# Performance work log

Measured on AMD Instinct MI355X. Metric: run time of the kernel, lower is better.

The kernel has to match this reference:

```python
import jax, jax.numpy as jnp
import numpy as np
import math

EPS = 1e-5  # BatchNorm eps; eval mode with running_mean=0, running_var=1


def maxpool(x, k, p):
    return jax.lax.reduce_window(x, -jnp.inf, jax.lax.max,
                                 (1, 1, k, k), (1, 1, 1, 1),
                                 ((0, 0), (0, 0), (p, p), (p, p)))


def conv1x1(x, w, b=None):
    # x: [B,Cin,H,W], w: [Cout,Cin]
    y = jnp.einsum('oi,bihw->bohw', w, x)
    if b is not None:
        y = y + b[None, :, None, None]
    return y


def bn_eval(x, g, b):
    scale = g / jnp.sqrt(1.0 + EPS)
    return x * scale[None, :, None, None] + b[None, :, None, None]


def setup_inputs() -> dict:
    B, C, H, W = 2, 64, 80, 80
    c1, c2, c3 = 21, 21, 22
    ch = 32  # C//2
    ks = jax.random.split(jax.random.key(0), 16)
    s = 0.05
    inp = {
        'x': jax.random.normal(ks[0], (B, C, H, W), jnp.float32),
        'q1_w': jax.random.normal(ks[1], (c1, c1), jnp.float32) * s,
        'q1_g': jnp.ones((c1,), jnp.float32),
        'q1_b': jnp.zeros((c1,), jnp.float32),
        'q2_w': jax.random.normal(ks[2], (c2, c2), jnp.float32) * s,
        'q2_g': jnp.ones((c2,), jnp.float32),
        'q2_b': jnp.zeros((c2,), jnp.float32),
        'q3_w': jax.random.normal(ks[3], (c3, c3), jnp.float32) * s,
        'q3_g': jnp.ones((c3,), jnp.float32),
        'q3_b': jnp.zeros((c3,), jnp.float32),
        'k_hf_w': jax.random.normal(ks[4], (ch, C), jnp.float32) * s,
        'k_hf_b': jnp.zeros((ch,), jnp.float32),
        'k_lf_w': jax.random.normal(ks[5], (C - ch, C), jnp.float32) * s,
        'k_lf_b': jnp.zeros((C - ch,), jnp.float32),
        'k_fuse_w': jax.random.normal(ks[6], (C, C), jnp.float32) * s,
        'k_fuse_b': jnp.zeros((C,), jnp.float32),
        'v_bn_g': jnp.ones((C,), jnp.float32),
        'v_bn_b': jnp.zeros((C,), jnp.float32),
        'v_w': jax.random.normal(ks[7], (C, C), jnp.float32) * s,
        'v_b': jnp.zeros((C,), jnp.float32),
        'out_w': jax.random.normal(ks[8], (C, C), jnp.float32) * s,
        'out_b': jnp.zeros((C,), jnp.float32),
    }
    return inp


def reference(x, q1_w, q1_g, q1_b, q2_w, q2_g, q2_b, q3_w, q3_g, q3_b,
              k_hf_w, k_hf_b, k_lf_w, k_lf_b, k_fuse_w, k_fuse_b,
              v_bn_g, v_bn_b, v_w, v_b, out_w, out_b):
    B, C, H, W = x.shape
    N = H * W
    c1 = q1_w.shape[0]
    c2 = q2_w.shape[0]
    # Q: ThreeGroupConvQ (split -> 1x1 conv (no bias) -> BN -> ReLU -> concat)
    x1, x2, x3 = jnp.split(x, [c1, c1 + c2], axis=1)
    y1 = jax.nn.relu(bn_eval(conv1x1(x1, q1_w), q1_g, q1_b))
    y2 = jax.nn.relu(bn_eval(conv1x1(x2, q2_w), q2_g, q2_b))
    y3 = jax.nn.relu(bn_eval(conv1x1(x3, q3_w), q3_g, q3_b))
    Q = jnp.concatenate([y1, y2, y3], axis=1)
    # K: ThermalStructureExtractor
    p3 = maxpool(x, 3, 1)
    p5 = maxpool(x, 5, 2)
    low = (p3 + p5) * 0.5
    high = conv1x1(x - low, k_hf_w, k_hf_b)
    lowp = conv1x1(low, k_lf_w, k_lf_b)
    K = conv1x1(jnp.concatenate([high, lowp], axis=1), k_fuse_w, k_fuse_b)
    # V: BN -> 1x1 conv
    V = conv1x1(bn_eval(x, v_bn_g, v_bn_b), v_w, v_b)
    # attention over N = H*W spatial tokens, channel features
    Qc = Q.reshape(B, C, N)
    Kc = K.reshape(B, C, N)
    Vc = V.reshape(B, C, N)
    attn = jax.nn.softmax(
        jnp.einsum('bcn,bcm->bnm', Qc, Kc) / math.sqrt(C), axis=-1)  # [B,N,N]
    out = jnp.einsum('bnm,bcm->bcn', attn, Vc).reshape(B, C, H, W)
    return conv1x1(out, out_w, out_b) + x
```

## Files before the change

### kernel.cpp

```cpp
#include <hip/hip_runtime.h>
#include <hip/hip_bf16.h>


#define BATCH 2
#define CH 64
#define HH 80
#define WW 80
#define NN 6400
#define NT 100
#define NG 4
#define KTPS 25
#define EPSV 1e-5f
#define NEGBIG (-1e30f)
#define QP 72
#define LOG2E8 0.18033688f
#define VSP 65
#define GREG 27648
#define OPF 65

typedef __hip_bfloat16 bf16;
typedef __attribute__((ext_vector_type(8))) short short8;
typedef __attribute__((ext_vector_type(4))) float f4;
#define MFMA16 __builtin_amdgcn_mfma_f32_16x16x32_bf16

__device__ __forceinline__ float b2f(bf16 v){ return __bfloat162float(v); }
__device__ __forceinline__ bf16 f2b(float v){ return __float2bfloat16(v); }
__device__ __forceinline__ ushort f2bu(float v){ return ((__hip_bfloat16_raw)__float2bfloat16(v)).x; }
__device__ __forceinline__ unsigned pkbf(float a, float b){
  union { __hip_bfloat162 h2; unsigned u; } cv;
  cv.h2 = __float22bfloat162_rn(make_float2(a, b));
  return cv.u;
}
__device__ __forceinline__ float fexp2(float x){
#if __has_builtin(__builtin_amdgcn_exp2f)
  return __builtin_amdgcn_exp2f(x);
#else
  return exp2f(x);
#endif
}

#define OFF_BIAS 0
#define OFF_WH_B 768
#define OFF_LOW_B (768 + 32768)
#define OFF_Q_B   (OFF_LOW_B + BATCH*CH*NN*2)
#define OFF_K_B   (OFF_Q_B   + BATCH*CH*NN*2)
#define OFF_V_B   (OFF_K_B   + BATCH*CH*NN*2)

__global__ __launch_bounds__(256) void setup_pool(
    const float* __restrict__ x,
    const float* __restrict__ q1w, const float* __restrict__ q1g, const float* __restrict__ q1b,
    const float* __restrict__ q2w, const float* __restrict__ q2g, const float* __restrict__ q2b,
    const float* __restrict__ q3w, const float* __restrict__ q3g, const float* __restrict__ q3b,
    const float* __restrict__ khw, const float* __restrict__ khb,
    const float* __restrict__ klw, const float* __restrict__ klb,
    const float* __restrict__ kfw, const float* __restrict__ kfb,
    const float* __restrict__ vg,  const float* __restrict__ vbnb,
    const float* __restrict__ vw,  const float* __restrict__ vb,
    const float* __restrict__ outw,
    float* __restrict__ biasf, bf16* __restrict__ wh, bf16* __restrict__ lowg)
{
  __shared__ float sbv[64];
  int tid = threadIdx.x;
  int blk = blockIdx.x;

  if (blk < 16) {
    float rs = rsqrtf(1.0f + EPSV);
    bf16* wq   = wh;
    bf16* wvp  = wh + 4096;
    bf16* wa1  = wh + 8192;
    bf16* wa2m = wh + 12288;

    int t = blk*256 + tid;
    int ci = t & 63, co = t >> 6;
    int o = ci*64 + co;

    float w = 0.f, g;
    if (co < 21)      { g = q1g[co];    w = (ci < 21)              ? q1w[co*21 + ci]            : 0.f; }
    else if (co < 42) { g = q2g[co-21]; w = (ci >= 21 && ci < 42)  ? q2w[(co-21)*21 + (ci-21)]  : 0.f; }
    else              { g = q3g[co-42]; w = (ci >= 42)             ? q3w[(co-42)*22 + (ci-42)]  : 0.f; }
    wq[o] = f2b(w * g * rs * LOG2E8);

    float a1 = 0.f, a2 = 0.f, av = 0.f;
    #pragma unroll 8
    for (int j = 0; j < 32; ++j) {
      a1 += kfw[co*64 + j]      * khw[j*64 + ci];
      a2 += kfw[co*64 + 32 + j] * klw[j*64 + ci];
    }
    #pragma unroll 8
    for (int j = 0; j < 64; ++j)
      av += outw[co*64 + j] * vw[j*64 + ci];
    wa1[o]  = f2b(a1);
    wa2m[o] = f2b(a2 - a1);
    wvp[o]  = f2b(av * vg[ci] * rs);

    if (blk == 0) {
      if (tid < 64) {
        int j = tid;
        float bvo = vb[j];
        for (int c2 = 0; c2 < 64; ++c2) bvo += vw[j*64 + c2] * vbnb[c2];
        sbv[j] = bvo;
      }
      __syncthreads();
      if (tid < 64) {
        int c2 = tid;
        float bq;
        if (c2 < 21)      bq = q1b[c2];
        else if (c2 < 42) bq = q2b[c2-21];
        else              bq = q3b[c2-42];
        biasf[c2] = bq * LOG2E8;
        float bk = kfb[c2];
        #pragma unroll 8
        for (int j = 0; j < 32; ++j) {
          bk += kfw[c2*64 + j]      * khb[j];
          bk += kfw[c2*64 + 32 + j] * klb[j];
        }
        biasf[64 + c2] = bk;
        float bvp = 0.f;
        #pragma unroll 8
        for (int j = 0; j < 64; ++j) bvp += outw[c2*64 + j] * sbv[j];
        biasf[128 + c2] = bvp;
      }
    }
  } else {
    int t4 = ((blk - 16)*256 + tid)*4;
    int bc = t4 / NN; int n = t4 % NN;
    int h = n / WW, w0 = n % WW;
    const float* p = x + bc*NN;
    float m5[4], m3[4];
    #pragma unroll
    for (int j=0;j<4;++j){ m5[j]=NEGBIG; m3[j]=NEGBIG; }
    #pragma unroll
    for (int dh = -2; dh <= 2; ++dh) {
      int hh = h + dh; if (hh < 0 || hh >= HH) continue;
      float r[12];
      const float* row = p + hh*WW;
      if (w0 >= 4)      { float4 a = *(const float4*)&row[w0-4]; r[0]=a.x;r[1]=a.y;r[2]=a.z;r[3]=a.w; }
      else              { r[0]=NEGBIG;r[1]=NEGBIG;r[2]=NEGBIG;r[3]=NEGBIG; }
      { float4 a = *(const float4*)&row[w0]; r[4]=a.x;r[5]=a.y;r[6]=a.z;r[7]=a.w; }
      if (w0 + 7 < WW)  { float4 a = *(const float4*)&row[w0+4]; r[8]=a.x;r[9]=a.y;r[10]=a.z;r[11]=a.w; }
      else              { r[8]=NEGBIG;r[9]=NEGBIG;r[10]=NEGBIG;r[11]=NEGBIG; }
      bool in3 = (dh >= -1 && dh <= 1);
      #pragma unroll
      for (int j=0;j<4;++j) {
        float v3 = fmaxf(fmaxf(r[3+j], r[4+j]), r[5+j]);
        float v5 = fmaxf(fmaxf(r[2+j], v3), r[6+j]);
        m5[j] = fmaxf(m5[j], v5);
        if (in3) m3[j] = fmaxf(m3[j], v3);
      }
    }
    ushort4 o;
    o.x = f2bu(0.5f*(m3[0]+m5[0]));
    o.y = f2bu(0.5f*(m3[1]+m5[1]));
    o.z = f2bu(0.5f*(m3[2]+m5[2]));
    o.w = f2bu(0.5f*(m3[3]+m5[3]));
    *(ushort4*)&lowg[t4] = o;
  }
}

__global__ __launch_bounds__(256) void qkv_kernel(
    const float* __restrict__ x, const float* __restrict__ biasf,
    const bf16* __restrict__ wh, const bf16* __restrict__ lowg,
    bf16* __restrict__ qgT, bf16* __restrict__ kgT, bf16* __restrict__ vgc)
{
  __shared__ __align__(16) float xs[64*32];
  __shared__ __align__(16) float lows[64*32];
  __shared__ __align__(16) bf16  wbuf[16384];
  __shared__ ushort vs[64*VSP];
  __shared__ float bias[192];

  int tid = threadIdx.x;
  int blk = blockIdx.x;
  int b = blk / (NT*2);
  int rem = blk % (NT*2);
  int tile = rem >> 1, half = rem & 1;
  int n0 = tile*64 + half*32;

  #pragma unroll
  for (int i = 0; i < 8; ++i) {
    int e = i*256 + tid; int c = e >> 5, p = e & 31;
    xs[c*32 + p]   = x[(b*CH + c)*NN + n0 + p];
    lows[c*32 + p] = b2f(lowg[(b*CH + c)*NN + n0 + p]);
  }
  #pragma unroll
  for (int i = 0; i < 16; ++i)
    ((uint2*)wbuf)[i*256 + tid] = ((const uint2*)wh)[i*256 + tid];
  if (tid < 192) bias[tid] = biasf[tid];
  __syncthreads();

  int co = tid & 63, pg = tid >> 6;
  const bf16* wq   = wbuf;
  const bf16* wvp  = wbuf + 4096;
  const bf16* wa1  = wbuf + 8192;
  const bf16* wa2m = wbuf + 12288;

  {
    float bq = bias[co];
    float4 a0 = make_float4(bq,bq,bq,bq), a1v = a0;
    for (int ci = 0; ci < 64; ++ci) {
      float wv = b2f(wq[ci*64 + co]);
      float4 x0 = *(const float4*)&xs[ci*32 + pg*8];
      float4 x1 = *(const float4*)&xs[ci*32 + pg*8 + 4];
      a0.x += wv*x0.x; a0.y += wv*x0.y; a0.z += wv*x0.z; a0.w += wv*x0.w;
      a1v.x += wv*x1.x; a1v.y += wv*x1.y; a1v.z += wv*x1.z; a1v.w += wv*x1.w;
    }
    float q8[8] = {a0.x,a0.y,a0.z,a0.w,a1v.x,a1v.y,a1v.z,a1v.w};
    #pragma unroll
    for (int j=0;j<8;++j)
      qgT[(size_t)(b*NN + n0 + pg*8 + j)*64 + co] = f2b(fmaxf(q8[j], 0.f));
  }
  {
    float bv = bias[128 + co];
    float4 a0 = make_float4(bv,bv,bv,bv), a1v = a0;
    for (int ci = 0; ci < 64; ++ci) {
      float wv = b2f(wvp[ci*64 + co]);
      float4 x0 = *(const float4*)&xs[ci*32 + pg*8];
      float4 x1 = *(const float4*)&xs[ci*32 + pg*8 + 4];
      a0.x += wv*x0.x; a0.y += wv*x0.y; a0.z += wv*x0.z; a0.w += wv*x0.w;
      a1v.x += wv*x1.x; a1v.y += wv*x1.y; a1v.z += wv*x1.z; a1v.w += wv*x1.w;
    }
    float v8[8] = {a0.x,a0.y,a0.z,a0.w,a1v.x,a1v.y,a1v.z,a1v.w};
    #pragma unroll
    for (int j=0;j<8;++j)
      vs[co*VSP + pg*8 + j] = f2bu(v8[j]);
  }
  __syncthreads();
  {
    int c = tid >> 2, cb = (tid & 3)*8;
    ushort u[8];
    #pragma unroll
    for (int j=0;j<8;++j) u[j] = vs[c*VSP + cb + j];
    uint4 pk;
    pk.x = (uint)u[0] | ((uint)u[1] << 16);
    pk.y = (uint)u[2] | ((uint)u[3] << 16);
    pk.z = (uint)u[4] | ((uint)u[5] << 16);
    pk.w = (uint)u[6] | ((uint)u[7] << 16);
    *(uint4*)&vgc[(size_t)(b*CH + c)*NN + n0 + cb] = pk;
  }
  {
    float bk = bias[64 + co];
    float4 a0 = make_float4(bk,bk,bk,bk), a1v = a0;
    for (int ci = 0; ci < 64; ++ci) {
      float w1 = b2f(wa1[ci*64 + co]);
      float w2 = b2f(wa2m[ci*64 + co]);
      float4 x0 = *(const float4*)&xs[ci*32 + pg*8];
      float4 x1 = *(const float4*)&xs[ci*32 + pg*8 + 4];
      float4 l0 = *(const float4*)&lows[ci*32 + pg*8];
      float4 l1 = *(const float4*)&lows[ci*32 + pg*8 + 4];
      a0.x += w1*x0.x + w2*l0.x; a0.y += w1*x0.y + w2*l0.y;
      a0.z += w1*x0.z + w2*l0.z; a0.w += w1*x0.w + w2*l0.w;
      a1v.x += w1*x1.x + w2*l1.x; a1v.y += w1*x1.y + w2*l1.y;
      a1v.z += w1*x1.z + w2*l1.z; a1v.w += w1*x1.w + w2*l1.w;
    }
    float k8[8] = {a0.x,a0.y,a0.z,a0.w,a1v.x,a1v.y,a1v.z,a1v.w};
    #pragma unroll
    for (int j=0;j<8;++j)
      kgT[(size_t)(b*NN + n0 + pg*8 + j)*64 + co] = f2b(k8[j]);
  }
}

__global__ __launch_bounds__(1024, 4) void attn_mono(
    const bf16* __restrict__ qgT, const bf16* __restrict__ kgT, const bf16* __restrict__ vgc,
    const float* __restrict__ x, const float* __restrict__ outb,
    float* __restrict__ out)
{
  __shared__ __align__(16) char sm[120064];
  bf16* Qld = (bf16*)sm;
  float* linv = (float*)(sm + 9216 + NG*GREG);

  int tid = threadIdx.x;
  int g  = tid >> 8;
  int gt = tid & 255;
  int b = blockIdx.x / NT, tile = blockIdx.x % NT;
  int n0 = tile*64;
  int wv = gt >> 6, lane = gt & 63, ln = lane & 15, quad = lane >> 4;
  int arow = (wv*16 + ln)*QP;

  char* gbase = sm + 9216 + g*GREG;
  bf16* Kld = (bf16*)gbase;
  bf16* Vld = (bf16*)(gbase + 9216);
  bf16* Pld = (bf16*)(gbase + 18432);

  {
    int f = tid*4; int n = f >> 6, c = f & 63;
    *(uint2*)&Qld[n*QP + c] = *(const uint2*)&qgT[(size_t)(b*NN + n0 + n)*64 + c];
  }
  __syncthreads();
  short8 bq[4][2];
  #pragma unroll
  for (int nt = 0; nt < 4; ++nt) {
    bq[nt][0] = *(const short8*)&Qld[(nt*16 + ln)*QP + quad*8];
    bq[nt][1] = *(const short8*)&Qld[(nt*16 + ln)*QP + 32 + quad*8];
  }

  f4 accO[4];
  float lacc[4];
  #pragma unroll
  for (int t=0;t<4;++t) accO[t] = (f4){0.f,0.f,0.f,0.f};
  #pragma unroll
  for (int nt=0;nt<4;++nt) lacc[nt] = 0.f;

  uint2 kreg[4], vreg[4];
  int mbase = g*KTPS*64;
  #pragma unroll
  for (int i = 0; i < 4; ++i) {
    int f = (i*256 + gt)*4; int rr = f >> 6, cc = f & 63;
    kreg[i] = *(const uint2*)&kgT[(size_t)(b*NN + mbase + rr)*64 + cc];
    vreg[i] = *(const uint2*)&vgc[(size_t)(b*CH + rr)*NN + mbase + cc];
  }

  for (int kt = 0; kt < KTPS; ++kt) {
    __syncthreads();
    #pragma unroll
    for (int i = 0; i < 4; ++i) {
      int f = (i*256 + gt)*4; int rr = f >> 6, cc = f & 63;
      *(uint2*)&Kld[rr*QP + cc] = kreg[i];
      *(uint2*)&Vld[rr*QP + cc] = vreg[i];
    }
    __syncthreads();
    if (kt + 1 < KTPS) {
      int m0 = mbase + (kt+1)*64;
      #pragma unroll
      for (int i = 0; i < 4; ++i) {
        int f = (i*256 + gt)*4; int rr = f >> 6, cc = f & 63;
        kreg[i] = *(const uint2*)&kgT[(size_t)(b*NN + m0 + rr)*64 + cc];
        vreg[i] = *(const uint2*)&vgc[(size_t)(b*CH + rr)*NN + m0 + cc];
      }
    }

    short8 ak0 = *(const short8*)&Kld[arow + quad*8];
    short8 ak1 = *(const short8*)&Kld[arow + 32 + quad*8];
    f4 accS[4];
    #pragma unroll
    for (int nt = 0; nt < 4; ++nt) {
      f4 z = (f4){0.f,0.f,0.f,0.f};
      z = MFMA16(ak0, bq[nt][0], z, 0, 0, 0);
      accS[nt] = MFMA16(ak1, bq[nt][1], z, 0, 0, 0);
    }
    #pragma unroll
    for (int nt = 0; nt < 4; ++nt) {
      float p0 = fexp2(accS[nt][0]), p1 = fexp2(accS[nt][1]);
      float p2 = fexp2(accS[nt][2]), p3 = fexp2(accS[nt][3]);
      lacc[nt] += (p0 + p1) + (p2 + p3);
      uint2 pk;
      pk.x = pkbf(p0, p1);
      pk.y = pkbf(p2, p3);
      *(uint2*)&Pld[(nt*16 + ln)*QP + wv*16 + quad*4] = pk;
    }
    __syncthreads();

    short8 ap0 = *(const short8*)&Pld[arow + quad*8];
    short8 ap1 = *(const short8*)&Pld[arow + 32 + quad*8];
    #pragma unroll
    for (int t = 0; t < 4; ++t) {
      short8 bv0 = *(const short8*)&Vld[(t*16+ln)*QP + quad*8];
      short8 bv1 = *(const short8*)&Vld[(t*16+ln)*QP + 32 + quad*8];
      accO[t] = MFMA16(ap0, bv0, accO[t], 0, 0, 0);
      accO[t] = MFMA16(ap1, bv1, accO[t], 0, 0, 0);
    }
  }

  __syncthreads();
  float* Og    = (float*)gbase;
  float* lgred = (float*)(gbase + 16896);
  #pragma unroll
  for (int t = 0; t < 4; ++t) {
    #pragma unroll
    for (int r = 0; r < 4; ++r)
      Og[(wv*16 + quad*4 + r)*OPF + t*16 + ln] = accO[t][r];
  }
  #pragma unroll
  for (int nt = 0; nt < 4; ++nt) {
    float s = lacc[nt];
    s += __shfl_xor(s, 16);
    s += __shfl_xor(s, 32);
    if (quad == 0) lgred[wv*64 + nt*16 + ln] = s;
  }
  __syncthreads();
  if (tid < 64) {
    float l = 0.f;
    #pragma unroll
    for (int g2 = 0; g2 < NG; ++g2) {
      const float* lr = (const float*)(sm + 9216 + g2*GREG + 16896);
      l += (lr[tid] + lr[64 + tid]) + (lr[128 + tid] + lr[192 + tid]);
    }
    linv[tid] = 1.0f / l;
  }
  __syncthreads();
  {
    int c = tid >> 4, q = tid & 15;
    int nl = q*4;
    float a0=0.f, a1=0.f, a2=0.f, a3=0.f;
    #pragma unroll
    for (int g2 = 0; g2 < NG; ++g2) {
      const float* og = (const float*)(sm + 9216 + g2*GREG);
      a0 += og[(nl+0)*OPF + c];
      a1 += og[(nl+1)*OPF + c];
      a2 += og[(nl+2)*OPF + c];
      a3 += og[(nl+3)*OPF + c];
    }
    size_t gidx = (size_t)(b*CH + c)*NN + n0 + nl;
    float4 xv = *(const float4*)&x[gidx];
    float bc = outb[c];
    float4 o;
    o.x = a0*linv[nl+0] + bc + xv.x;
    o.y = a1*linv[nl+1] + bc + xv.y;
    o.z = a2*linv[nl+2] + bc + xv.z;
    o.w = a3*linv[nl+3] + bc + xv.w;
    *(float4*)&out[gidx] = o;
  }
}

extern "C" void kernel_launch(void* const* d_in, const int* in_sizes, int n_in,
                              void* d_out, int out_size, void* d_ws, size_t ws_size,
                              hipStream_t stream) {
  const float* x    = (const float*)d_in[0];
  const float* q1w  = (const float*)d_in[1];
  const float* q1g  = (const float*)d_in[2];
  const float* q1b  = (const float*)d_in[3];
  const float* q2w  = (const float*)d_in[4];
  const float* q2g  = (const float*)d_in[5];
  const float* q2b  = (const float*)d_in[6];
  const float* q3w  = (const float*)d_in[7];
  const float* q3g  = (const float*)d_in[8];
  const float* q3b  = (const float*)d_in[9];
  const float* khw  = (const float*)d_in[10];
  const float* khb  = (const float*)d_in[11];
  const float* klw  = (const float*)d_in[12];
  const float* klb  = (const float*)d_in[13];
  const float* kfw  = (const float*)d_in[14];
  const float* kfb  = (const float*)d_in[15];
  const float* vbg  = (const float*)d_in[16];
  const float* vbb  = (const float*)d_in[17];
  const float* vw   = (const float*)d_in[18];
  const float* vb   = (const float*)d_in[19];
  const float* outw = (const float*)d_in[20];
  const float* outb = (const float*)d_in[21];

  char*   wsb  = (char*)d_ws;
  float*  biasf= (float*)(wsb + OFF_BIAS);
  bf16*   wh   = (bf16*)(wsb + OFF_WH_B);
  bf16*   lowg = (bf16*)(wsb + OFF_LOW_B);
  bf16*   qgT  = (bf16*)(wsb + OFF_Q_B);
  bf16*   kgT  = (bf16*)(wsb + OFF_K_B);
  bf16*   vgc  = (bf16*)(wsb + OFF_V_B);

  hipLaunchKernelGGL(setup_pool, dim3(16 + BATCH*CH*NN/1024), dim3(256), 0, stream,
                     x, q1w,q1g,q1b,q2w,q2g,q2b,q3w,q3g,q3b,
                     khw,khb,klw,klb,kfw,kfb,vbg,vbb,vw,vb,outw,
                     biasf, wh, lowg);
  hipLaunchKernelGGL(qkv_kernel, dim3(BATCH*NT*2), dim3(256), 0, stream,
                     x, biasf, wh, lowg, qgT, kgT, vgc);
  hipLaunchKernelGGL(attn_mono, dim3(BATCH*NT), dim3(1024), 0, stream,
                     qgT, kgT, vgc, x, outb, (float*)d_out);
}
```

Measured before the change: 178.7 us.

## Split attention into split-K partial kernel and separate reduction kernel

Replaces the monolithic attention kernel (200 blocks of 1024 threads, four in-block KV groups) with a split-K scheme. There are 1000 blocks of 512 threads, each handling 128 queries against one tenth of the keys, and each writes bf16 partial outputs and row sums to workspace. A new reduce kernel sums the partials, normalizes, and adds bias and residual. The goal is better CU occupancy and parallelism on MI355X and less shared memory per block. The cost is an extra launch, global round-trip traffic for partials, and extra bf16 rounding of the partial accumulators.

```diff
diff --git a/kernel.cpp b/kernel.cpp
--- a/kernel.cpp
+++ b/kernel.cpp
@@ -8,15 +8,14 @@
 #define WW 80
 #define NN 6400
 #define NT 100
-#define NG 4
-#define KTPS 25
+#define NT2 50
+#define KS 10
+#define KTPS (NT/KS)
 #define EPSV 1e-5f
 #define NEGBIG (-1e30f)
 #define QP 72
 #define LOG2E8 0.18033688f
 #define VSP 65
-#define GREG 27648
-#define OPF 65
 
 typedef __hip_bfloat16 bf16;
 typedef __attribute__((ext_vector_type(8))) short short8;
@@ -26,6 +25,9 @@
 __device__ __forceinline__ float b2f(bf16 v){ return __bfloat162float(v); }
 __device__ __forceinline__ bf16 f2b(float v){ return __float2bfloat16(v); }
 __device__ __forceinline__ ushort f2bu(float v){ return ((__hip_bfloat16_raw)__float2bfloat16(v)).x; }
+__device__ __forceinline__ float bu2f(ushort u){
+  union { unsigned int i; float f; } w; w.i = ((unsigned int)u) << 16; return w.f;
+}
 __device__ __forceinline__ unsigned pkbf(float a, float b){
   union { __hip_bfloat162 h2; unsigned u; } cv;
   cv.h2 = __float22bfloat162_rn(make_float2(a, b));
@@ -45,6 +47,8 @@
 #define OFF_Q_B   (OFF_LOW_B + BATCH*CH*NN*2)
 #define OFF_K_B   (OFF_Q_B   + BATCH*CH*NN*2)
 #define OFF_V_B   (OFF_K_B   + BATCH*CH*NN*2)
+#define OFF_P_B   (OFF_V_B   + BATCH*CH*NN*2)
+#define OFF_ML_B  (OFF_P_B   + BATCH*NT2*KS*8192*2)
 
 __global__ __launch_bounds__(256) void setup_pool(
     const float* __restrict__ x,
@@ -258,38 +262,39 @@
   }
 }
 
-__global__ __launch_bounds__(1024, 4) void attn_mono(
+__global__ __launch_bounds__(512, 8) void attn_partial(
     const bf16* __restrict__ qgT, const bf16* __restrict__ kgT, const bf16* __restrict__ vgc,
-    const float* __restrict__ x, const float* __restrict__ outb,
-    float* __restrict__ out)
+    ushort* __restrict__ part, float* __restrict__ pml)
 {
-  __shared__ __align__(16) char sm[120064];
-  bf16* Qld = (bf16*)sm;
-  float* linv = (float*)(sm + 9216 + NG*GREG);
+  __shared__ __align__(16) char smem[36864];
+  __shared__ float lred[512];
+  bf16* Qld = (bf16*)smem;
+  bf16* Pld = (bf16*)smem;
+  bf16* Kld = (bf16*)(smem + 18432);
+  bf16* Vld = (bf16*)(smem + 27648);
 
   int tid = threadIdx.x;
-  int g  = tid >> 8;
-  int gt = tid & 255;
-  int b = blockIdx.x / NT, tile = blockIdx.x % NT;
-  int n0 = tile*64;
-  int wv = gt >> 6, lane = gt & 63, ln = lane & 15, quad = lane >> 4;
-  int arow = (wv*16 + ln)*QP;
-
-  char* gbase = sm + 9216 + g*GREG;
-  bf16* Kld = (bf16*)gbase;
-  bf16* Vld = (bf16*)(gbase + 9216);
-  bf16* Pld = (bf16*)(gbase + 18432);
-
-  {
-    int f = tid*4; int n = f >> 6, c = f & 63;
+  int blk = blockIdx.x;
+  int b = blk / (NT2*KS);
+  int rem = blk % (NT2*KS);
+  int st = rem / KS, split = rem % KS;
+  int n0 = st*128;
+  int wv = tid >> 6, lane = tid & 63, ln = lane & 15, quad = lane >> 4;
+  int nh = wv >> 2, ms = wv & 3;
+  int arowK = (ms*16 + ln)*QP;
+  int arowP = (wv*16 + ln)*QP;
+
+  #pragma unroll
+  for (int i = 0; i < 4; ++i) {
+    int f = (i*512 + tid)*4; int n = f >> 6, c = f & 63;
     *(uint2*)&Qld[n*QP + c] = *(const uint2*)&qgT[(size_t)(b*NN + n0 + n)*64 + c];
   }
   __syncthreads();
   short8 bq[4][2];
   #pragma unroll
   for (int nt = 0; nt < 4; ++nt) {
-    bq[nt][0] = *(const short8*)&Qld[(nt*16 + ln)*QP + quad*8];
-    bq[nt][1] = *(const short8*)&Qld[(nt*16 + ln)*QP + 32 + quad*8];
+    bq[nt][0] = *(const short8*)&Qld[(nh*64 + nt*16 + ln)*QP + quad*8];
+    bq[nt][1] = *(const short8*)&Qld[(nh*64 + nt*16 + ln)*QP + 32 + quad*8];
   }
 
   f4 accO[4];
@@ -299,11 +304,11 @@
   #pragma unroll
   for (int nt=0;nt<4;++nt) lacc[nt] = 0.f;
 
-  uint2 kreg[4], vreg[4];
-  int mbase = g*KTPS*64;
-  #pragma unroll
-  for (int i = 0; i < 4; ++i) {
-    int f = (i*256 + gt)*4; int rr = f >> 6, cc = f & 63;
+  uint2 kreg[2], vreg[2];
+  int mbase = split*KTPS*64;
+  #pragma unroll
+  for (int i = 0; i < 2; ++i) {
+    int f = (i*512 + tid)*4; int rr = f >> 6, cc = f & 63;
     kreg[i] = *(const uint2*)&kgT[(size_t)(b*NN + mbase + rr)*64 + cc];
     vreg[i] = *(const uint2*)&vgc[(size_t)(b*CH + rr)*NN + mbase + cc];
   }
@@ -311,8 +316,8 @@
   for (int kt = 0; kt < KTPS; ++kt) {
     __syncthreads();
     #pragma unroll
-    for (int i = 0; i < 4; ++i) {
-      int f = (i*256 + gt)*4; int rr = f >> 6, cc = f & 63;
+    for (int i = 0; i < 2; ++i) {
+      int f = (i*512 + tid)*4; int rr = f >> 6, cc = f & 63;
       *(uint2*)&Kld[rr*QP + cc] = kreg[i];
       *(uint2*)&Vld[rr*QP + cc] = vreg[i];
     }
@@ -320,15 +325,15 @@
     if (kt + 1 < KTPS) {
       int m0 = mbase + (kt+1)*64;
       #pragma unroll
-      for (int i = 0; i < 4; ++i) {
-        int f = (i*256 + gt)*4; int rr = f >> 6, cc = f & 63;
+      for (int i = 0; i < 2; ++i) {
+        int f = (i*512 + tid)*4; int rr = f >> 6, cc = f & 63;
         kreg[i] = *(const uint2*)&kgT[(size_t)(b*NN + m0 + rr)*64 + cc];
         vreg[i] = *(const uint2*)&vgc[(size_t)(b*CH + rr)*NN + m0 + cc];
       }
     }
 
-    short8 ak0 = *(const short8*)&Kld[arow + quad*8];
-    short8 ak1 = *(const short8*)&Kld[arow + 32 + quad*8];
+    short8 ak0 = *(const short8*)&Kld[arowK + quad*8];
+    short8 ak1 = *(const short8*)&Kld[arowK + 32 + quad*8];
     f4 accS[4];
     #pragma unroll
     for (int nt = 0; nt < 4; ++nt) {
@@ -344,12 +349,12 @@
       uint2 pk;
       pk.x = pkbf(p0, p1);
       pk.y = pkbf(p2, p3);
-      *(uint2*)&Pld[(nt*16 + ln)*QP + wv*16 + quad*4] = pk;
+      *(uint2*)&Pld[(nh*64 + nt*16 + ln)*QP + ms*16 + quad*4] = pk;
     }
     __syncthreads();
 
-    short8 ap0 = *(const short8*)&Pld[arow + quad*8];
-    short8 ap1 = *(const short8*)&Pld[arow + 32 + quad*8];
+    short8 ap0 = *(const short8*)&Pld[arowP + quad*8];
+    short8 ap1 = *(const short8*)&Pld[arowP + 32 + quad*8];
     #pragma unroll
     for (int t = 0; t < 4; ++t) {
       short8 bv0 = *(const short8*)&Vld[(t*16+ln)*QP + quad*8];
@@ -359,48 +364,71 @@
     }
   }
 
-  __syncthreads();
-  float* Og    = (float*)gbase;
-  float* lgred = (float*)(gbase + 16896);
+  size_t pbase = ((size_t)(b*NT2 + st)*KS + split)*8192;
+  ushort* pp = part + pbase;
   #pragma unroll
   for (int t = 0; t < 4; ++t) {
-    #pragma unroll
-    for (int r = 0; r < 4; ++r)
-      Og[(wv*16 + quad*4 + r)*OPF + t*16 + ln] = accO[t][r];
+    uint2 pk;
+    pk.x = pkbf(accO[t][0], accO[t][1]);
+    pk.y = pkbf(accO[t][2], accO[t][3]);
+    *(uint2*)&pp[(size_t)(t*16 + ln)*128 + wv*16 + quad*4] = pk;
   }
   #pragma unroll
   for (int nt = 0; nt < 4; ++nt) {
     float s = lacc[nt];
     s += __shfl_xor(s, 16);
     s += __shfl_xor(s, 32);
-    if (quad == 0) lgred[wv*64 + nt*16 + ln] = s;
+    if (quad == 0) lred[wv*64 + nt*16 + ln] = s;
   }
   __syncthreads();
-  if (tid < 64) {
+  if (tid < 128) {
+    int nh2 = tid >> 6, j = tid & 63;
+    float l = (lred[(nh2*4+0)*64 + j] + lred[(nh2*4+1)*64 + j])
+            + (lred[(nh2*4+2)*64 + j] + lred[(nh2*4+3)*64 + j]);
+    size_t mlb = ((size_t)(b*NT2 + st)*KS + split)*128;
+    pml[mlb + tid] = l;
+  }
+}
+
+__global__ __launch_bounds__(256) void attn_reduce(
+    const ushort* __restrict__ part, const float* __restrict__ pml,
+    const float* __restrict__ x, const float* __restrict__ outb,
+    float* __restrict__ out)
+{
+  __shared__ float linv[128];
+  __shared__ float ob[64];
+
+  int tid = threadIdx.x;
+  int blk = blockIdx.x;
+  int b = blk / (NT2*2);
+  int rem = blk % (NT2*2);
+  int st = rem >> 1, half = rem & 1;
+  size_t base = (size_t)(b*NT2 + st)*KS;
+
+  if (tid < 128) {
     float l = 0.f;
     #pragma unroll
-    for (int g2 = 0; g2 < NG; ++g2) {
-      const float* lr = (const float*)(sm + 9216 + g2*GREG + 16896);
-      l += (lr[tid] + lr[64 + tid]) + (lr[128 + tid] + lr[192 + tid]);
-    }
+    for (int s=0;s<KS;++s) l += pml[(base+s)*128 + tid];
     linv[tid] = 1.0f / l;
   }
+  if (tid >= 128 && tid < 192) ob[tid-128] = outb[tid-128];
   __syncthreads();
-  {
-    int c = tid >> 4, q = tid & 15;
+
+  #pragma unroll
+  for (int j = 0; j < 4; ++j) {
+    int idx = j*256 + tid;
+    int c = half*32 + (idx >> 5), q = idx & 31;
+    float a0=0.f, a1=0.f, a2=0.f, a3=0.f;
+    #pragma unroll
+    for (int s = 0; s < KS; ++s) {
+      uint2 v = *(const uint2*)&part[(base+s)*8192 + (size_t)c*128 + q*4];
+      a0 += bu2f((ushort)(v.x & 0xffff)); a1 += bu2f((ushort)(v.x >> 16));
+      a2 += bu2f((ushort)(v.y & 0xffff)); a3 += bu2f((ushort)(v.y >> 16));
+    }
     int nl = q*4;
-    float a0=0.f, a1=0.f, a2=0.f, a3=0.f;
-    #pragma unroll
-    for (int g2 = 0; g2 < NG; ++g2) {
-      const float* og = (const float*)(sm + 9216 + g2*GREG);
-      a0 += og[(nl+0)*OPF + c];
-      a1 += og[(nl+1)*OPF + c];
-      a2 += og[(nl+2)*OPF + c];
-      a3 += og[(nl+3)*OPF + c];
-    }
-    size_t gidx = (size_t)(b*CH + c)*NN + n0 + nl;
+    size_t gidx = (size_t)(b*CH + c)*NN + st*128 + nl;
     float4 xv = *(const float4*)&x[gidx];
-    float bc = outb[c];
+    float bc = ob[c];
     float4 o;
     o.x = a0*linv[nl+0] + bc + xv.x;
     o.y = a1*linv[nl+1] + bc + xv.y;
@@ -443,6 +471,8 @@
   bf16*   qgT  = (bf16*)(wsb + OFF_Q_B);
   bf16*   kgT  = (bf16*)(wsb + OFF_K_B);
   bf16*   vgc  = (bf16*)(wsb + OFF_V_B);
+  ushort* part = (ushort*)(wsb + OFF_P_B);
+  float*  pml  = (float*)(wsb + OFF_ML_B);
 
   hipLaunchKernelGGL(setup_pool, dim3(16 + BATCH*CH*NN/1024), dim3(256), 0, stream,
                      x, q1w,q1g,q1b,q2w,q2g,q2b,q3w,q3g,q3b,
@@ -450,6 +480,8 @@
                      biasf, wh, lowg);
   hipLaunchKernelGGL(qkv_kernel, dim3(BATCH*NT*2), dim3(256), 0, stream,
                      x, biasf, wh, lowg, qgT, kgT, vgc);
-  hipLaunchKernelGGL(attn_mono, dim3(BATCH*NT), dim3(1024), 0, stream,
-                     qgT, kgT, vgc, x, outb, (float*)d_out);
-}
+  hipLaunchKernelGGL(attn_partial, dim3(BATCH*NT2*KS), dim3(512), 0, stream,
+                     qgT, kgT, vgc, part, pml);
+  hipLaunchKernelGGL(attn_reduce, dim3(BATCH*NT2*2), dim3(256), 0, stream,
+                     part, pml, x, outb, (float*)d_out);
+}
```

After: 445.7 us. +149.5%, slower.
